# Optimization experiments

Hardware: AMD Instinct MI355X
Metric: run time of the kernel (lower is better)

The kernel has to match this reference:

```python
import jax, jax.numpy as jnp
import numpy as np


def _curvature_kernel():
    w = np.array([[-1/16, 5/16, -1/16],
                  [ 5/16, -1.0,  5/16],
                  [-1/16, 5/16, -1/16]], dtype=np.float32)
    return jnp.asarray(w)[None, None]  # OIHW = (1,1,3,3)


def setup_inputs() -> dict:
    key = jax.random.key(0)
    B, N, H, W = 32, 512, 64, 64
    x = jax.random.normal(key, (B, N, H, W), dtype=jnp.float32)
    weight = _curvature_kernel()
    k = 256  # int(ratio * N) with ratio = 0.5
    return {"x": x, "weight": weight, "k": k}


def reference(x, weight, k):
    B, N, H, W = x.shape
    # Per-(batch, candidate) single-channel 3x3 VALID conv (edge/curvature filter)
    xr = x.reshape(B * N, 1, H, W)
    out = jax.lax.conv_general_dilated(
        xr, weight, window_strides=(1, 1), padding='VALID',
        dimension_numbers=('NCHW', 'OIHW', 'NCHW'))  # (B*N,1,H-2,W-2)
    # abs + full spatial reduction -> score per candidate
    p = jnp.abs(out).sum(axis=(1, 2, 3)).reshape(B, N)
    _, idx = jax.lax.top_k(p, k)  # (B, k)
    # batched gather of top-k candidates along the N axis
    return jnp.take_along_axis(x, idx[:, :, None, None], axis=1)  # (B,k,H,W)
```

## Files before the change

kernel.cpp:

```cpp
#include <hip/hip_runtime.h>

#define BATCH 32
#define NCAND 512
#define HH 64
#define WW 64
#define KSEL 256
#define HW (HH * WW)
#define OUT_H (HH - 2)
#define OUT_W (WW - 2)
#define NOUT (OUT_H * OUT_W)

__global__ __launch_bounds__(256) void score_kernel(
    const float* __restrict__ x, const float* __restrict__ w,
    double* __restrict__ p) {
  __shared__ float tile[HH][WW];
  __shared__ double partial[4];

  const int img = blockIdx.x;
  const int tid = threadIdx.x;

  const float4* src4 = (const float4*)(x + (size_t)img * HW);
  float4* t4 = (float4*)&tile[0][0];
#pragma unroll
  for (int i = 0; i < 4; ++i) t4[i * 256 + tid] = src4[i * 256 + tid];

  const double w00 = w[0], w01 = w[1], w02 = w[2];
  const double w10 = w[3], w11 = w[4], w12 = w[5];
  const double w20 = w[6], w21 = w[7], w22 = w[8];

  __syncthreads();

  double acc = 0.0;
#pragma unroll
  for (int it = 0; it < 16; ++it) {
    const int o = it * 256 + tid;
    if (o < NOUT) {
      const int i = o / OUT_W;
      const int j = o - i * OUT_W;
      double s;
      s  = (double)tile[i    ][j] * w00 + (double)tile[i    ][j + 1] * w01 + (double)tile[i    ][j + 2] * w02;
      s += (double)tile[i + 1][j] * w10 + (double)tile[i + 1][j + 1] * w11 + (double)tile[i + 1][j + 2] * w12;
      s += (double)tile[i + 2][j] * w20 + (double)tile[i + 2][j + 1] * w21 + (double)tile[i + 2][j + 2] * w22;
      acc += fabs(s);
    }
  }

#pragma unroll
  for (int off = 32; off > 0; off >>= 1) acc += __shfl_down(acc, off, 64);
  if ((tid & 63) == 0) partial[tid >> 6] = acc;
  __syncthreads();
  if (tid == 0) p[img] = partial[0] + partial[1] + partial[2] + partial[3];
}

__global__ __launch_bounds__(512) void rank_kernel(
    const double* __restrict__ p, int* __restrict__ idx) {
  __shared__ double sp[NCAND];
  const int b = blockIdx.x;
  const int n = threadIdx.x;
  sp[n] = p[(size_t)b * NCAND + n];
  __syncthreads();
  const double pn = sp[n];
  int rank = 0;
#pragma unroll 8
  for (int m = 0; m < NCAND; ++m) {
    const double pm = sp[m];
    rank += (pm > pn) || (pm == pn && m < n);
  }
  if (rank < KSEL) idx[b * KSEL + rank] = n;
}

__global__ __launch_bounds__(256) void gather_kernel(
    const float* __restrict__ x, const int* __restrict__ idx,
    float* __restrict__ out) {
  const int o = blockIdx.x;
  const int b = o / KSEL;
  const int n = idx[o];
  const float4* src = (const float4*)(x + ((size_t)b * NCAND + n) * HW);
  float4* dst = (float4*)(out + (size_t)o * HW);
  const int tid = threadIdx.x;
#pragma unroll
  for (int i = 0; i < 4; ++i) dst[i * 256 + tid] = src[i * 256 + tid];
}

extern "C" void kernel_launch(void* const* d_in, const int* in_sizes, int n_in,
                              void* d_out, int out_size, void* d_ws,
                              size_t ws_size, hipStream_t stream) {
  const float* x = (const float*)d_in[0];
  const float* w = (const float*)d_in[1];
  float* out = (float*)d_out;

  double* p = (double*)d_ws;
  int* idx = (int*)(p + BATCH * NCAND);

  score_kernel<<<BATCH * NCAND, 256, 0, stream>>>(x, w, p);
  rank_kernel<<<BATCH, 512, 0, stream>>>(p, idx);
  gather_kernel<<<BATCH * KSEL, 256, 0, stream>>>(x, idx, out);
}
```

Before: 444.2 us.

## Exploit stencil symmetry with sliding-row partial sums in score kernel

Restructures the 3x3 stencil so each wave handles a 16-row strip and each lane one column. Horizontal partial sums per row are reused as the window slides down the strip. The kernel's row and column symmetry is exploited, so only four weights are used (w[0], w[1], w[3], w[4]), which cuts the double-precision multiplies per output. The cost being removed is FP64 FMA count and the per-output index division. The risk is that results are only correct for symmetric filter weights, and the summation order changes slightly.

```diff
diff --git a/kernel.cpp b/kernel.cpp
--- a/kernel.cpp
+++ b/kernel.cpp
@@ -8,46 +8,68 @@
 #define HW (HH * WW)
 #define OUT_H (HH - 2)
 #define OUT_W (WW - 2)
-#define NOUT (OUT_H * OUT_W)
 
 __global__ __launch_bounds__(256) void score_kernel(
     const float* __restrict__ x, const float* __restrict__ w,
     double* __restrict__ p) {
-  __shared__ float tile[HH][WW];
+  __shared__ float tile[HW];
   __shared__ double partial[4];
 
   const int img = blockIdx.x;
   const int tid = threadIdx.x;
 
   const float4* src4 = (const float4*)(x + (size_t)img * HW);
-  float4* t4 = (float4*)&tile[0][0];
+  float4* t4 = (float4*)tile;
 #pragma unroll
   for (int i = 0; i < 4; ++i) t4[i * 256 + tid] = src4[i * 256 + tid];
 
-  const double w00 = w[0], w01 = w[1], w02 = w[2];
-  const double w10 = w[3], w11 = w[4], w12 = w[5];
-  const double w20 = w[6], w21 = w[7], w22 = w[8];
+  const double wa0 = (double)w[0];
+  const double wa1 = (double)w[1];
+  const double wb0 = (double)w[3];
+  const double wb1 = (double)w[4];
 
   __syncthreads();
 
+  const int wave = tid >> 6;
+  const int lane = tid & 63;
+  const int j = lane < OUT_W ? lane : (OUT_W - 1);
+  const int i0 = wave * 16;
+  const int nout = (wave == 3) ? 14 : 16;
+  const float* tj = tile + i0 * WW + j;
+
   double acc = 0.0;
+
+  double Ai, Ai1, Bi1;
+  {
+    float f0 = tj[0], f1 = tj[1], f2 = tj[2];
+    double h = (double)f0 + (double)f2, m = (double)f1;
+    Ai = fma(h, wa0, m * wa1);
+  }
+  {
+    float f0 = tj[WW], f1 = tj[WW + 1], f2 = tj[WW + 2];
+    double h = (double)f0 + (double)f2, m = (double)f1;
+    Ai1 = fma(h, wa0, m * wa1);
+    Bi1 = fma(h, wb0, m * wb1);
+  }
 #pragma unroll
-  for (int it = 0; it < 16; ++it) {
-    const int o = it * 256 + tid;
-    if (o < NOUT) {
-      const int i = o / OUT_W;
-      const int j = o - i * OUT_W;
-      double s;
-      s  = (double)tile[i    ][j] * w00 + (double)tile[i    ][j + 1] * w01 + (double)tile[i    ][j + 2] * w02;
-      s += (double)tile[i + 1][j] * w10 + (double)tile[i + 1][j + 1] * w11 + (double)tile[i + 1][j + 2] * w12;
-      s += (double)tile[i + 2][j] * w20 + (double)tile[i + 2][j + 1] * w21 + (double)tile[i + 2][j + 2] * w22;
+  for (int r = 0; r < 16; ++r) {
+    if (r < nout) {
+      const float* row = tj + (r + 2) * WW;
+      float f0 = row[0], f1 = row[1], f2 = row[2];
+      double h = (double)f0 + (double)f2, m = (double)f1;
+      double A2 = fma(h, wa0, m * wa1);
+      double B2 = fma(h, wb0, m * wb1);
+      double s = Ai + Bi1 + A2;
       acc += fabs(s);
+      Ai = Ai1; Ai1 = A2; Bi1 = B2;
     }
   }
 
+  if (lane >= OUT_W) acc = 0.0;
+
 #pragma unroll
   for (int off = 32; off > 0; off >>= 1) acc += __shfl_down(acc, off, 64);
-  if ((tid & 63) == 0) partial[tid >> 6] = acc;
+  if (lane == 0) partial[wave] = acc;
   __syncthreads();
   if (tid == 0) p[img] = partial[0] + partial[1] + partial[2] + partial[3];
 }
```

Result: no change. 435.8 us (-1.9%).
